# Optimization experiments

Measured on AMD Instinct MI355X. Metric: run time of the kernel, lower is better.

The kernel has to match this reference:

```python
import jax, jax.numpy as jnp
from jax import lax
import numpy as np

H = 256

def _cell(x, h, c, wih, whh, bih, bhh):
    # PyTorch LSTMCell: gates ordered i, f, g, o
    g = x @ wih.T + bih + h @ whh.T + bhh
    i, f, gg, o = jnp.split(g, 4, axis=-1)
    c = jax.nn.sigmoid(f) * c + jax.nn.sigmoid(i) * jnp.tanh(gg)
    h = jax.nn.sigmoid(o) * jnp.tanh(c)
    return h, c


def setup_inputs() -> dict:
    key = jax.random.key(0)
    ks = iter(jax.random.split(key, 64))
    def lin(out_f, in_f):
        s = 1.0 / np.sqrt(in_f)
        w = jax.random.uniform(next(ks), (out_f, in_f), minval=-s, maxval=s, dtype=jnp.float32)
        b = jax.random.uniform(next(ks), (out_f,), minval=-s, maxval=s, dtype=jnp.float32)
        return w, b
    def cellp():
        s = 1.0 / np.sqrt(H)
        return tuple(jax.random.uniform(next(ks), sh, minval=-s, maxval=s, dtype=jnp.float32)
                     for sh in [(4 * H, H), (4 * H, H), (4 * H,), (4 * H,)])
    d = {}
    d['x'] = jax.random.normal(next(ks), (20, 256, 64, 64), dtype=jnp.float32)
    d['fc_en1_w'], d['fc_en1_b'] = lin(1024, 4096)
    d['fc_en2_w'], d['fc_en2_b'] = lin(H, 1024)
    for nm in ['en1', 'en2', 'en3', 'de1', 'de2', 'de3']:
        d[nm + '_wih'], d[nm + '_whh'], d[nm + '_bih'], d[nm + '_bhh'] = cellp()
    d['fc_de1_w'], d['fc_de1_b'] = lin(1024, H)
    d['fc_de2_w'], d['fc_de2_b'] = lin(4096, 1024)
    d['future_step'] = 10
    return d


def reference(x, fc_en1_w, fc_en1_b, fc_en2_w, fc_en2_b,
              en1_wih, en1_whh, en1_bih, en1_bhh,
              en2_wih, en2_whh, en2_bih, en2_bhh,
              en3_wih, en3_whh, en3_bih, en3_bhh,
              de1_wih, de1_whh, de1_bih, de1_bhh,
              de2_wih, de2_whh, de2_bih, de2_bhh,
              de3_wih, de3_whh, de3_bih, de3_bhh,
              fc_de1_w, fc_de1_b, fc_de2_w, fc_de2_b, future_step):
    seq, B = x.shape[0], x.shape[1]
    xf = x.reshape(seq, B, -1)  # (S, B, 4096)
    z0 = jnp.zeros((B, H), x.dtype)

    def enc_step(carry, xt):
        h1, c1, h2, c2, h3, c3 = carry
        z = jax.nn.relu(xt @ fc_en1_w.T + fc_en1_b)
        z = jax.nn.relu(z @ fc_en2_w.T + fc_en2_b)
        h1, c1 = _cell(z, h1, c1, en1_wih, en1_whh, en1_bih, en1_bhh)
        h2, c2 = _cell(h1, h2, c2, en2_wih, en2_whh, en2_bih, en2_bhh)
        h3, c3 = _cell(h2, h3, c3, en3_wih, en3_whh, en3_bih, en3_bhh)
        return (h1, c1, h2, c2, h3, c3), None

    enc_carry, _ = lax.scan(enc_step, (z0,) * 6, xf)
    h_e3 = enc_carry[4]

    def dec_step(carry, _):
        h1, c1, h2, c2, h3, c3 = carry
        h1, c1 = _cell(z0, h1, c1, de1_wih, de1_whh, de1_bih, de1_bhh)
        h2, c2 = _cell(h1, h2, c2, de2_wih, de2_whh, de2_bih, de2_bhh)
        h3, c3 = _cell(h2, h3, c3, de3_wih, de3_whh, de3_bih, de3_bhh)
        y = jax.nn.relu(h3 @ fc_de1_w.T + fc_de1_b)
        y = jnp.tanh(y @ fc_de2_w.T + fc_de2_b)
        return (h1, c1, h2, c2, h3, c3), y

    _, ys = lax.scan(dec_step, (h_e3, z0, z0, z0, z0, z0), None, length=future_step)
    return ys.reshape(future_step, B, 64, 64)
```

## Files before the change

kernel.cpp:

```cpp
#include <hip/hip_runtime.h>
#include <math.h>

static __device__ __forceinline__ float sigf(float v) { return 1.0f / (1.0f + expf(-v)); }

using s8v = __attribute__((ext_vector_type(8))) short;
using f4v = __attribute__((ext_vector_type(4))) float;

static __device__ __forceinline__ void splitf(float f, unsigned short& h, unsigned short& l) {
  unsigned u = __float_as_uint(f);
  unsigned short hb = (unsigned short)((u + 0x7FFFu + ((u >> 16) & 1u)) >> 16);
  float hf = __uint_as_float(((unsigned)hb) << 16);
  float lf = f - hf;
  unsigned ul = __float_as_uint(lf);
  unsigned short lb = (unsigned short)((ul + 0x7FFFu + ((ul >> 16) & 1u)) >> 16);
  h = hb; l = lb;
}

static __device__ __forceinline__ void splitf4(float4 a, uint2& hOut, uint2& lOut) {
  unsigned hxy, hzw;
  asm("v_cvt_pk_bf16_f32 %0, %1, %2" : "=v"(hxy) : "v"(a.x), "v"(a.y));
  asm("v_cvt_pk_bf16_f32 %0, %1, %2" : "=v"(hzw) : "v"(a.z), "v"(a.w));
  float hx = __uint_as_float(hxy << 16);
  float hy = __uint_as_float(hxy & 0xFFFF0000u);
  float hz = __uint_as_float(hzw << 16);
  float hw = __uint_as_float(hzw & 0xFFFF0000u);
  unsigned lxy, lzw;
  asm("v_cvt_pk_bf16_f32 %0, %1, %2" : "=v"(lxy) : "v"(a.x - hx), "v"(a.y - hy));
  asm("v_cvt_pk_bf16_f32 %0, %1, %2" : "=v"(lzw) : "v"(a.z - hz), "v"(a.w - hw));
  hOut.x = hxy; hOut.y = hzw;
  lOut.x = lxy; lOut.y = lzw;
}

struct WsplitArgs {
  const float* W[4];
  unsigned short* WH[4];
  unsigned short* WL[4];
};
__global__ __launch_bounds__(256) void wsplit4(WsplitArgs a)
{
  int blk = blockIdx.x;
  int seg, base;
  if (blk < 4096)      { seg = 0; base = blk; }
  else if (blk < 4352) { seg = 1; base = blk - 4096; }
  else if (blk < 4608) { seg = 2; base = blk - 4352; }
  else                 { seg = 3; base = blk - 4608; }
  int i = base * 256 + threadIdx.x;
  float4 v = ((const float4*)a.W[seg])[i];
  ushort4 h, l;
  splitf(v.x, h.x, l.x); splitf(v.y, h.y, l.y);
  splitf(v.z, h.z, l.z); splitf(v.w, h.w, l.w);
  ((ushort4*)a.WH[seg])[i] = h;
  ((ushort4*)a.WL[seg])[i] = l;
}

template <int OSPLIT>
__global__ __launch_bounds__(256) void gemm_sf(
    const float* __restrict__ A,
    const unsigned short* __restrict__ WH, const unsigned short* __restrict__ WL,
    const float* __restrict__ bias, float* __restrict__ C,
    unsigned short* __restrict__ OH, unsigned short* __restrict__ OL,
    int M, int N, int K, int act)
{
  __shared__ unsigned short AsH[128 * 40];
  __shared__ unsigned short AsL[128 * 40];
  __shared__ unsigned short WsH[64 * 40];
  __shared__ unsigned short WsL[64 * 40];

  const int t = threadIdx.x;
  const int w = t >> 6, lane = t & 63;
  const int lrow = lane & 15, lk = (lane >> 4) * 8;
  const int m0 = blockIdx.x * 128, n0 = blockIdx.y * 64;

  f4v acc[2][4];
#pragma unroll
  for (int i = 0; i < 2; ++i)
#pragma unroll
    for (int j = 0; j < 4; ++j) acc[i][j] = (f4v){0.f, 0.f, 0.f, 0.f};

  for (int k0 = 0; k0 < K; k0 += 32) {
#pragma unroll
    for (int i = 0; i < 4; ++i) {
      int v = i * 256 + t;
      int row = v >> 3, kq = (v & 7) << 2;
      float4 a = *(const float4*)(A + (size_t)(m0 + row) * K + k0 + kq);
      uint2 h2, l2;
      splitf4(a, h2, l2);
      *(uint2*)&AsH[row * 40 + kq] = h2;
      *(uint2*)&AsL[row * 40 + kq] = l2;
    }
    {
      int row = t >> 2, q = (t & 3) * 8;
      *(s8v*)&WsH[row * 40 + q] = *(const s8v*)(WH + (size_t)(n0 + row) * K + k0 + q);
      *(s8v*)&WsL[row * 40 + q] = *(const s8v*)(WL + (size_t)(n0 + row) * K + k0 + q);
    }
    __syncthreads();

    s8v aH[2], aL[2], bH[4], bL[4];
#pragma unroll
    for (int mt = 0; mt < 2; ++mt) {
      int r = (w * 32 + mt * 16 + lrow) * 40 + lk;
      aH[mt] = *(const s8v*)&AsH[r];
      aL[mt] = *(const s8v*)&AsL[r];
    }
#pragma unroll
    for (int nt = 0; nt < 4; ++nt) {
      int r = (nt * 16 + lrow) * 40 + lk;
      bH[nt] = *(const s8v*)&WsH[r];
      bL[nt] = *(const s8v*)&WsL[r];
    }
#pragma unroll
    for (int mt = 0; mt < 2; ++mt)
#pragma unroll
      for (int nt = 0; nt < 4; ++nt) {
        acc[mt][nt] = __builtin_amdgcn_mfma_f32_16x16x32_bf16(aH[mt], bH[nt], acc[mt][nt], 0, 0, 0);
        acc[mt][nt] = __builtin_amdgcn_mfma_f32_16x16x32_bf16(aH[mt], bL[nt], acc[mt][nt], 0, 0, 0);
        acc[mt][nt] = __builtin_amdgcn_mfma_f32_16x16x32_bf16(aL[mt], bH[nt], acc[mt][nt], 0, 0, 0);
      }
    __syncthreads();
  }

#pragma unroll
  for (int mt = 0; mt < 2; ++mt)
#pragma unroll
    for (int nt = 0; nt < 4; ++nt) {
      int gcol = n0 + nt * 16 + lrow;
      float bv = bias[gcol];
#pragma unroll
      for (int r = 0; r < 4; ++r) {
        int grow = m0 + w * 32 + mt * 16 + (lane >> 4) * 4 + r;
        float v = acc[mt][nt][r] + bv;
        if (act == 1) v = fmaxf(v, 0.f);
        else if (act == 2) v = tanhf(v);
        if (OSPLIT) {
          unsigned short h, l;
          splitf(v, h, l);
          OH[(size_t)grow * N + gcol] = h;
          OL[(size_t)grow * N + gcol] = l;
        } else {
          C[(size_t)grow * N + gcol] = v;
        }
      }
    }
}

template <int OSPLIT>
__global__ __launch_bounds__(256) void gemm_bb(
    const unsigned short* __restrict__ AH, const unsigned short* __restrict__ AL,
    const unsigned short* __restrict__ WH, const unsigned short* __restrict__ WL,
    const float* __restrict__ bias, float* __restrict__ C,
    unsigned short* __restrict__ OH, unsigned short* __restrict__ OL,
    int M, int N, int K, int act)
{
  __shared__ unsigned short AsH[128 * 40];
  __shared__ unsigned short AsL[128 * 40];
  __shared__ unsigned short WsH[64 * 40];
  __shared__ unsigned short WsL[64 * 40];

  const int t = threadIdx.x;
  const int w = t >> 6, lane = t & 63;
  const int lrow = lane & 15, lk = (lane >> 4) * 8;
  const int m0 = blockIdx.x * 128, n0 = blockIdx.y * 64;

  f4v acc[2][4];
#pragma unroll
  for (int i = 0; i < 2; ++i)
#pragma unroll
    for (int j = 0; j < 4; ++j) acc[i][j] = (f4v){0.f, 0.f, 0.f, 0.f};

  for (int k0 = 0; k0 < K; k0 += 32) {
#pragma unroll
    for (int i = 0; i < 2; ++i) {
      int v = i * 256 + t;
      int row = v >> 2, q = (v & 3) * 8;
      *(s8v*)&AsH[row * 40 + q] = *(const s8v*)(AH + (size_t)(m0 + row) * K + k0 + q);
      *(s8v*)&AsL[row * 40 + q] = *(const s8v*)(AL + (size_t)(m0 + row) * K + k0 + q);
    }
    {
      int row = t >> 2, q = (t & 3) * 8;
      *(s8v*)&WsH[row * 40 + q] = *(const s8v*)(WH + (size_t)(n0 + row) * K + k0 + q);
      *(s8v*)&WsL[row * 40 + q] = *(const s8v*)(WL + (size_t)(n0 + row) * K + k0 + q);
    }
    __syncthreads();

    s8v aH[2], aL[2], bH[4], bL[4];
#pragma unroll
    for (int mt = 0; mt < 2; ++mt) {
      int r = (w * 32 + mt * 16 + lrow) * 40 + lk;
      aH[mt] = *(const s8v*)&AsH[r];
      aL[mt] = *(const s8v*)&AsL[r];
    }
#pragma unroll
    for (int nt = 0; nt < 4; ++nt) {
      int r = (nt * 16 + lrow) * 40 + lk;
      bH[nt] = *(const s8v*)&WsH[r];
      bL[nt] = *(const s8v*)&WsL[r];
    }
#pragma unroll
    for (int mt = 0; mt < 2; ++mt)
#pragma unroll
      for (int nt = 0; nt < 4; ++nt) {
        acc[mt][nt] = __builtin_amdgcn_mfma_f32_16x16x32_bf16(aH[mt], bH[nt], acc[mt][nt], 0, 0, 0);
        acc[mt][nt] = __builtin_amdgcn_mfma_f32_16x16x32_bf16(aH[mt], bL[nt], acc[mt][nt], 0, 0, 0);
        acc[mt][nt] = __builtin_amdgcn_mfma_f32_16x16x32_bf16(aL[mt], bH[nt], acc[mt][nt], 0, 0, 0);
      }
    __syncthreads();
  }

#pragma unroll
  for (int mt = 0; mt < 2; ++mt)
#pragma unroll
    for (int nt = 0; nt < 4; ++nt) {
      int gcol = n0 + nt * 16 + lrow;
      float bv = bias[gcol];
#pragma unroll
      for (int r = 0; r < 4; ++r) {
        int grow = m0 + w * 32 + mt * 16 + (lane >> 4) * 4 + r;
        float v = acc[mt][nt][r] + bv;
        if (act == 1) v = fmaxf(v, 0.f);
        else if (act == 2) v = tanhf(v);
        if (OSPLIT) {
          unsigned short h, l;
          splitf(v, h, l);
          OH[(size_t)grow * N + gcol] = h;
          OL[(size_t)grow * N + gcol] = l;
        } else {
          C[(size_t)grow * N + gcol] = v;
        }
      }
    }
}

struct PrepArgs {
  const float* wih[6];
  const float* whh[6];
  const float* bih[6];
  const float* bhh[6];
  float* wihP;
  float* whhP;
  float* bP;
};
__global__ __launch_bounds__(256) void prep_pack6(PrepArgs a)
{
  const int l = blockIdx.y;
  const int j = blockIdx.x, k = threadIdx.x;
  const float* wih = a.wih[l];
  const float* whh = a.whh[l];
  float* wihP = a.wihP + (size_t)l * 262144;
  float* whhP = a.whhP + (size_t)l * 262144;
  float4 v, c;
  v.x = wih[(0 * 256 + j) * 256 + k];
  v.y = wih[(1 * 256 + j) * 256 + k];
  v.z = wih[(2 * 256 + j) * 256 + k];
  v.w = wih[(3 * 256 + j) * 256 + k];
  *(float4*)&wihP[((size_t)j * 256 + k) * 4] = v;
  c.x = whh[(0 * 256 + j) * 256 + k];
  c.y = whh[(1 * 256 + j) * 256 + k];
  c.z = whh[(2 * 256 + j) * 256 + k];
  c.w = whh[(3 * 256 + j) * 256 + k];
  *(float4*)&whhP[((size_t)j * 256 + k) * 4] = c;
  if (k < 4)
    a.bP[l * 1024 + j * 4 + k] = a.bih[l][k * 256 + j] + a.bhh[l][k * 256 + j];
}

__global__ __launch_bounds__(256) void transpose256(
    const float* __restrict__ in, float* __restrict__ out)
{
  const int t = blockIdx.x, c4 = blockIdx.y;
  const int r = threadIdx.x;
  float4 v = *(const float4*)(in + ((size_t)t * 256 + r) * 256 + c4 * 4);
  float* op = out + (size_t)t * 65536 + (size_t)(c4 * 4) * 256 + r;
  op[0]   = v.x;
  op[256] = v.y;
  op[512] = v.z;
  op[768] = v.w;
}

__global__ __launch_bounds__(256) void transpose256s(
    const float* __restrict__ in, unsigned short* __restrict__ outH,
    unsigned short* __restrict__ outL)
{
  const int t = blockIdx.x, c4 = blockIdx.y;
  const int r = threadIdx.x;
  float4 v = *(const float4*)(in + ((size_t)t * 256 + r) * 256 + c4 * 4);
  ushort4 h, l;
  splitf(v.x, h.x, l.x); splitf(v.y, h.y, l.y);
  splitf(v.z, h.z, l.z); splitf(v.w, h.w, l.w);
  size_t o = (size_t)t * 65536 + (size_t)(c4 * 4) * 256 + r;
  outH[o] = h.x; outH[o + 256] = h.y; outH[o + 512] = h.z; outH[o + 768] = h.w;
  outL[o] = l.x; outL[o + 256] = l.y; outL[o + 512] = l.z; outL[o + 768] = l.w;
}

struct CellSlot {
  const float* x;
  const float* wih;
  const float* whh;
  const float* bias;
  const float* hin;
  float* c;
  float* hout;
  float* hcopy;
  int hasx;
};
struct CellArgs { CellSlot s[3]; };

__global__ __launch_bounds__(512) void cell_multi(CellArgs args)
{
  __shared__ float part[4][64][4];
  const CellSlot S = args.s[blockIdx.x >> 8];
  const int inner = blockIdx.x & 255;
  const int jg = inner & 63, bg = inner >> 6;
  const int t = threadIdx.x;
  const int lane = t & 63;
  const int wave = t >> 6;
  const int jwv = wave & 3;
  const int kh = __builtin_amdgcn_readfirstlane(wave >> 2);
  const int b = bg * 64 + lane;

  const int jw = __builtin_amdgcn_readfirstlane(jg * 4 + jwv);
  const float4* wh = (const float4*)(S.whh + (size_t)jw * 1024) + kh * 128;
  const float4* wi = (const float4*)(S.wih + (size_t)jw * 1024) + kh * 128;
  const float* hcol = S.hin + (size_t)kh * 128 * 256 + b;

  float4 acc;
  if (kh == 0) acc = *(const float4*)(S.bias + jw * 4);
  else         acc = (float4){0.f, 0.f, 0.f, 0.f};

  if (S.hasx) {
    const float* xcol = S.x + (size_t)kh * 128 * 256 + b;
#pragma unroll 8
    for (int k = 0; k < 128; ++k) {
      const float hv = hcol[k * 256];
      const float4 wv = wh[k];
      acc.x = fmaf(hv, wv.x, acc.x);
      acc.y = fmaf(hv, wv.y, acc.y);
      acc.z = fmaf(hv, wv.z, acc.z);
      acc.w = fmaf(hv, wv.w, acc.w);
      const float xv = xcol[k * 256];
      const float4 vv = wi[k];
      acc.x = fmaf(xv, vv.x, acc.x);
      acc.y = fmaf(xv, vv.y, acc.y);
      acc.z = fmaf(xv, vv.z, acc.z);
      acc.w = fmaf(xv, vv.w, acc.w);
    }
  } else {
#pragma unroll 8
    for (int k = 0; k < 128; ++k) {
      const float hv = hcol[k * 256];
      const float4 wv = wh[k];
      acc.x = fmaf(hv, wv.x, acc.x);
      acc.y = fmaf(hv, wv.y, acc.y);
      acc.z = fmaf(hv, wv.z, acc.z);
      acc.w = fmaf(hv, wv.w, acc.w);
    }
  }

  if (kh == 1) *(float4*)&part[jwv][lane][0] = acc;
  __syncthreads();
  if (kh == 0) {
    const float4 p = *(const float4*)&part[jwv][lane][0];
    acc.x += p.x; acc.y += p.y; acc.z += p.z; acc.w += p.w;

    const int idx = jw * 256 + b;
    const float cold = S.c[idx];
    const float ig = sigf(acc.x), fg = sigf(acc.y);
    const float gg = tanhf(acc.z), og = sigf(acc.w);
    const float cn = fg * cold + ig * gg;
    const float hn = og * tanhf(cn);
    S.c[idx] = cn;
    S.hout[idx] = hn;
    if (S.hcopy) S.hcopy[idx] = hn;
  }
}


extern "C" void kernel_launch(void* const* d_in, const int* in_sizes, int n_in,
                              void* d_out, int out_size, void* d_ws, size_t ws_size,
                              hipStream_t stream)
{
  const float* x_in  = (const float*)d_in[0];
  const float* w_en1 = (const float*)d_in[1];
  const float* b_en1 = (const float*)d_in[2];
  const float* w_en2 = (const float*)d_in[3];
  const float* b_en2 = (const float*)d_in[4];
  const float* cw[6][4];
  for (int i = 0; i < 6; ++i)
    for (int j = 0; j < 4; ++j) cw[i][j] = (const float*)d_in[5 + i * 4 + j];
  const float* w_de1 = (const float*)d_in[29];
  const float* b_de1 = (const float*)d_in[30];
  const float* w_de2 = (const float*)d_in[31];
  const float* b_de2 = (const float*)d_in[32];
  float* out = (float*)d_out;

  float* fs   = (float*)d_ws;
  float* wihP = fs;
  float* whhP = wihP + 6 * 262144;
  float* bP   = whhP + 6 * 262144;
  float* hb   = bP + 6 * 1024;
  float* cb   = hb + 12 * 65536;
  float* H3T  = cb + 6 * 65536;
  float* z2   = H3T + 10 * 65536;
  float* z2T  = z2 + 1310720;
  unsigned short* us = (unsigned short*)(z2T + 1310720);
  unsigned short* WEN1H = us;              us += 4194304;
  unsigned short* WEN1L = us;              us += 4194304;
  unsigned short* WEN2H = us;              us += 262144;
  unsigned short* WEN2L = us;              us += 262144;
  unsigned short* WDE1H = us;              us += 262144;
  unsigned short* WDE1L = us;              us += 262144;
  unsigned short* WDE2H = us;              us += 4194304;
  unsigned short* WDE2L = us;              us += 4194304;
  unsigned short* Z1H   = us;              us += 5242880;
  unsigned short* Z1L   = us;              us += 5242880;
  unsigned short* H3H = Z1H;
  unsigned short* H3L = Z1H + 655360;
  unsigned short* Y1H = Z1H + 1310720;
  unsigned short* Y1L = Z1H + 1310720 + 2621440;

  PrepArgs pa;
  for (int i = 0; i < 6; ++i) {
    pa.wih[i] = cw[i][0]; pa.whh[i] = cw[i][1];
    pa.bih[i] = cw[i][2]; pa.bhh[i] = cw[i][3];
  }
  pa.wihP = wihP; pa.whhP = whhP; pa.bP = bP;
  prep_pack6<<<dim3(256, 6), 256, 0, stream>>>(pa);

  WsplitArgs wa;
  wa.W[0] = w_en1; wa.WH[0] = WEN1H; wa.WL[0] = WEN1L;
  wa.W[1] = w_en2; wa.WH[1] = WEN2H; wa.WL[1] = WEN2L;
  wa.W[2] = w_de1; wa.WH[2] = WDE1H; wa.WL[2] = WDE1L;
  wa.W[3] = w_de2; wa.WH[3] = WDE2H; wa.WL[3] = WDE2L;
  wsplit4<<<8704, 256, 0, stream>>>(wa);
  hipMemsetAsync(hb, 0, (size_t)18 * 65536 * sizeof(float), stream);

  gemm_sf<1><<<dim3(40, 16), 256, 0, stream>>>(
      x_in, WEN1H, WEN1L, b_en1, nullptr, Z1H, Z1L, 5120, 1024, 4096, 1);
  gemm_bb<0><<<dim3(40, 4), 256, 0, stream>>>(
      Z1H, Z1L, WEN2H, WEN2L, b_en2, z2, nullptr, nullptr, 5120, 256, 1024, 1);
  transpose256<<<dim3(20, 64), 256, 0, stream>>>(z2, z2T);

  int pp[6] = {0, 0, 0, 0, 0, 0};
  auto HBuf = [&](int l, int p) { return hb + (size_t)(l * 2 + p) * 65536; };
  auto CBuf = [&](int l) { return cb + (size_t)l * 65536; };
  auto WI = [&](int l) { return wihP + (size_t)l * 262144; };
  auto WHp = [&](int l) { return whhP + (size_t)l * 262144; };
  auto BB = [&](int l) { return bP + (size_t)l * 1024; };

  for (int s = 0; s <= 21; ++s) {
    CellArgs a; int n = 0; int tog[3]; int nt = 0;
    if (s < 20) {
      a.s[n++] = {z2T + (size_t)s * 65536, WI(0), WHp(0), BB(0),
                  HBuf(0, pp[0]), CBuf(0), HBuf(0, pp[0] ^ 1), nullptr, 1};
      tog[nt++] = 0;
    }
    if (s >= 1 && s <= 20) {
      a.s[n++] = {HBuf(0, pp[0]), WI(1), WHp(1), BB(1),
                  HBuf(1, pp[1]), CBuf(1), HBuf(1, pp[1] ^ 1), nullptr, 1};
      tog[nt++] = 1;
    }
    if (s >= 2) {
      a.s[n++] = {HBuf(1, pp[1]), WI(2), WHp(2), BB(2),
                  HBuf(2, pp[2]), CBuf(2), HBuf(2, pp[2] ^ 1), nullptr, 1};
      tog[nt++] = 2;
    }
    cell_multi<<<n * 256, 512, 0, stream>>>(a);
    for (int i = 0; i < nt; ++i) pp[tog[i]] ^= 1;
  }

  for (int s = 0; s <= 11; ++s) {
    CellArgs a; int n = 0; int tog[3]; int nt = 0;
    if (s < 10) {
      const float* h1in = (s == 0) ? HBuf(2, pp[2]) : HBuf(3, pp[3]);
      a.s[n++] = {nullptr, WI(3), WHp(3), BB(3),
                  h1in, CBuf(3), HBuf(3, pp[3] ^ 1), nullptr, 0};
      tog[nt++] = 3;
    }
    if (s >= 1 && s <= 10) {
      a.s[n++] = {HBuf(3, pp[3]), WI(4), WHp(4), BB(4),
                  HBuf(4, pp[4]), CBuf(4), HBuf(4, pp[4] ^ 1), nullptr, 1};
      tog[nt++] = 4;
    }
    if (s >= 2) {
      a.s[n++] = {HBuf(4, pp[4]), WI(5), WHp(5), BB(5),
                  HBuf(5, pp[5]), CBuf(5), HBuf(5, pp[5] ^ 1),
                  H3T + (size_t)(s - 2) * 65536, 1};
      tog[nt++] = 5;
    }
    cell_multi<<<n * 256, 512, 0, stream>>>(a);
    for (int i = 0; i < nt; ++i) pp[tog[i]] ^= 1;
  }

  transpose256s<<<dim3(10, 64), 256, 0, stream>>>(H3T, H3H, H3L);
  gemm_bb<1><<<dim3(20, 16), 256, 0, stream>>>(
      H3H, H3L, WDE1H, WDE1L, b_de1, nullptr, Y1H, Y1L, 2560, 1024, 256, 1);
  gemm_bb<0><<<dim3(20, 64), 256, 0, stream>>>(
      Y1H, Y1L, WDE2H, WDE2L, b_de2, out, nullptr, nullptr, 2560, 4096, 1024, 2);

  (void)in_sizes; (void)n_in; (void)out_size; (void)ws_size;
}
```

Before: 844.5 us.

## Run LSTM cell recurrences on split-bf16 MFMA with concatenated weights

Replaces the scalar FP32 FMA LSTM cell kernel with an MFMA-based kernel that multiplies a concatenated [Whh|Wih] bf16 hi/lo split weight matrix against hi/lo split hidden/input states, emulating FP32 precision with three bf16 MFMAs. Hidden states are now stored as bf16 hi/lo pairs in batch-major layout, which removes the separate transpose kernels and lets the encoder fc2 output feed the cells directly. The intent is to cut the per-step latency of the 34 sequential cell launches by using matrix cores. The trade-off is that the launch now uses only 32 blocks per layer, which leaves most of the GPU idle, and the three-term split drops the lo*lo product, so precision is slightly lower.

Measured after the change: 933.3 us. 1.11x slower.

```diff
diff --git a/kernel.cpp b/kernel.cpp
--- a/kernel.cpp
+++ b/kernel.cpp
@@ -53,6 +53,37 @@
   ((ushort4*)a.WL[seg])[i] = l;
 }
 
+struct PrepArgs {
+  const float* wih[6];
+  const float* whh[6];
+  const float* bih[6];
+  const float* bhh[6];
+  unsigned short* WcatH;
+  unsigned short* WcatL;
+  float* bP;
+};
+__global__ __launch_bounds__(256) void prep_cat6(PrepArgs a)
+{
+  const int l = blockIdx.y;
+  const int j = blockIdx.x, k = threadIdx.x;
+  unsigned short* WH = a.WcatH + (size_t)l * 524288;
+  unsigned short* WL = a.WcatL + (size_t)l * 524288;
+#pragma unroll
+  for (int s = 0; s < 4; ++s) {
+    unsigned short h, lo;
+    float wh = a.whh[l][(s * 256 + j) * 256 + k];
+    splitf(wh, h, lo);
+    WH[(size_t)(j * 4 + s) * 512 + k] = h;
+    WL[(size_t)(j * 4 + s) * 512 + k] = lo;
+    float wi = a.wih[l][(s * 256 + j) * 256 + k];
+    splitf(wi, h, lo);
+    WH[(size_t)(j * 4 + s) * 512 + 256 + k] = h;
+    WL[(size_t)(j * 4 + s) * 512 + 256 + k] = lo;
+  }
+  if (k < 4)
+    a.bP[l * 1024 + j * 4 + k] = a.bih[l][k * 256 + j] + a.bhh[l][k * 256 + j];
+}
+
 template <int OSPLIT>
 __global__ __launch_bounds__(256) void gemm_sf(
     const float* __restrict__ A,
@@ -230,145 +261,129 @@
     }
 }
 
-struct PrepArgs {
-  const float* wih[6];
-  const float* whh[6];
-  const float* bih[6];
-  const float* bhh[6];
-  float* wihP;
-  float* whhP;
-  float* bP;
+struct CSlot {
+  const unsigned short* wH;
+  const unsigned short* wL;
+  const float* bias;
+  const unsigned short* xH;
+  const unsigned short* xL;
+  const unsigned short* hH;
+  const unsigned short* hL;
+  float* c;
+  unsigned short* oH;
+  unsigned short* oL;
+  unsigned short* h3H;
+  unsigned short* h3L;
+  int h3off;
+  int K;
 };
-__global__ __launch_bounds__(256) void prep_pack6(PrepArgs a)
+struct CArgs { CSlot s[3]; };
+
+__global__ __launch_bounds__(256) void cell_mfma(CArgs args)
 {
-  const int l = blockIdx.y;
-  const int j = blockIdx.x, k = threadIdx.x;
-  const float* wih = a.wih[l];
-  const float* whh = a.whh[l];
-  float* wihP = a.wihP + (size_t)l * 262144;
-  float* whhP = a.whhP + (size_t)l * 262144;
-  float4 v, c;
-  v.x = wih[(0 * 256 + j) * 256 + k];
-  v.y = wih[(1 * 256 + j) * 256 + k];
-  v.z = wih[(2 * 256 + j) * 256 + k];
-  v.w = wih[(3 * 256 + j) * 256 + k];
-  *(float4*)&wihP[((size_t)j * 256 + k) * 4] = v;
-  c.x = whh[(0 * 256 + j) * 256 + k];
-  c.y = whh[(1 * 256 + j) * 256 + k];
-  c.z = whh[(2 * 256 + j) * 256 + k];
-  c.w = whh[(3 * 256 + j) * 256 + k];
-  *(float4*)&whhP[((size_t)j * 256 + k) * 4] = c;
-  if (k < 4)
-    a.bP[l * 1024 + j * 4 + k] = a.bih[l][k * 256 + j] + a.bhh[l][k * 256 + j];
-}
-
-__global__ __launch_bounds__(256) void transpose256(
-    const float* __restrict__ in, float* __restrict__ out)
-{
-  const int t = blockIdx.x, c4 = blockIdx.y;
-  const int r = threadIdx.x;
-  float4 v = *(const float4*)(in + ((size_t)t * 256 + r) * 256 + c4 * 4);
-  float* op = out + (size_t)t * 65536 + (size_t)(c4 * 4) * 256 + r;
-  op[0]   = v.x;
-  op[256] = v.y;
-  op[512] = v.z;
-  op[768] = v.w;
-}
-
-__global__ __launch_bounds__(256) void transpose256s(
-    const float* __restrict__ in, unsigned short* __restrict__ outH,
-    unsigned short* __restrict__ outL)
-{
-  const int t = blockIdx.x, c4 = blockIdx.y;
-  const int r = threadIdx.x;
-  float4 v = *(const float4*)(in + ((size_t)t * 256 + r) * 256 + c4 * 4);
-  ushort4 h, l;
-  splitf(v.x, h.x, l.x); splitf(v.y, h.y, l.y);
-  splitf(v.z, h.z, l.z); splitf(v.w, h.w, l.w);
-  size_t o = (size_t)t * 65536 + (size_t)(c4 * 4) * 256 + r;
-  outH[o] = h.x; outH[o + 256] = h.y; outH[o + 512] = h.z; outH[o + 768] = h.w;
-  outL[o] = l.x; outL[o + 256] = l.y; outL[o + 512] = l.z; outL[o + 768] = l.w;
-}
-
-struct CellSlot {
-  const float* x;
-  const float* wih;
-  const float* whh;
-  const float* bias;
-  const float* hin;
-  float* c;
-  float* hout;
-  float* hcopy;
-  int hasx;
-};
-struct CellArgs { CellSlot s[3]; };
-
-__global__ __launch_bounds__(512) void cell_multi(CellArgs args)
-{
-  __shared__ float part[4][64][4];
-  const CellSlot S = args.s[blockIdx.x >> 8];
-  const int inner = blockIdx.x & 255;
-  const int jg = inner & 63, bg = inner >> 6;
+  __shared__ unsigned short AsH[128 * 40];
+  __shared__ unsigned short AsL[128 * 40];
+  __shared__ unsigned short WsH[64 * 40];
+  __shared__ unsigned short WsL[64 * 40];
+  __shared__ unsigned short tH[64 * 34];
+  __shared__ unsigned short tL[64 * 34];
+
+  const CSlot S = args.s[blockIdx.x >> 5];
+  const int inner = blockIdx.x & 31;
+  const int m0 = (inner >> 2) * 128, n0 = (inner & 3) * 64;
   const int t = threadIdx.x;
-  const int lane = t & 63;
-  const int wave = t >> 6;
-  const int jwv = wave & 3;
-  const int kh = __builtin_amdgcn_readfirstlane(wave >> 2);
-  const int b = bg * 64 + lane;
-
-  const int jw = __builtin_amdgcn_readfirstlane(jg * 4 + jwv);
-  const float4* wh = (const float4*)(S.whh + (size_t)jw * 1024) + kh * 128;
-  const float4* wi = (const float4*)(S.wih + (size_t)jw * 1024) + kh * 128;
-  const float* hcol = S.hin + (size_t)kh * 128 * 256 + b;
-
-  float4 acc;
-  if (kh == 0) acc = *(const float4*)(S.bias + jw * 4);
-  else         acc = (float4){0.f, 0.f, 0.f, 0.f};
-
-  if (S.hasx) {
-    const float* xcol = S.x + (size_t)kh * 128 * 256 + b;
-#pragma unroll 8
-    for (int k = 0; k < 128; ++k) {
-      const float hv = hcol[k * 256];
-      const float4 wv = wh[k];
-      acc.x = fmaf(hv, wv.x, acc.x);
-      acc.y = fmaf(hv, wv.y, acc.y);
-      acc.z = fmaf(hv, wv.z, acc.z);
-      acc.w = fmaf(hv, wv.w, acc.w);
-      const float xv = xcol[k * 256];
-      const float4 vv = wi[k];
-      acc.x = fmaf(xv, vv.x, acc.x);
-      acc.y = fmaf(xv, vv.y, acc.y);
-      acc.z = fmaf(xv, vv.z, acc.z);
-      acc.w = fmaf(xv, vv.w, acc.w);
-    }
-  } else {
-#pragma unroll 8
-    for (int k = 0; k < 128; ++k) {
-      const float hv = hcol[k * 256];
-      const float4 wv = wh[k];
-      acc.x = fmaf(hv, wv.x, acc.x);
-      acc.y = fmaf(hv, wv.y, acc.y);
-      acc.z = fmaf(hv, wv.z, acc.z);
-      acc.w = fmaf(hv, wv.w, acc.w);
-    }
-  }
-
-  if (kh == 1) *(float4*)&part[jwv][lane][0] = acc;
+  const int w = t >> 6, lane = t & 63;
+  const int lrow = lane & 15, lk = (lane >> 4) * 8;
+
+  f4v acc[2][4];
+#pragma unroll
+  for (int i = 0; i < 2; ++i)
+#pragma unroll
+    for (int j = 0; j < 4; ++j) acc[i][j] = (f4v){0.f, 0.f, 0.f, 0.f};
+
+  for (int k0 = 0; k0 < S.K; k0 += 32) {
+#pragma unroll
+    for (int i = 0; i < 2; ++i) {
+      int v = i * 256 + t;
+      int row = v >> 2, q = (v & 3) * 8;
+      *(s8v*)&AsH[row * 40 + q] = *(const s8v*)(S.wH + (size_t)(m0 + row) * 512 + k0 + q);
+      *(s8v*)&AsL[row * 40 + q] = *(const s8v*)(S.wL + (size_t)(m0 + row) * 512 + k0 + q);
+    }
+    {
+      const unsigned short* bh = (k0 < 256) ? (S.hH + k0) : (S.xH + (k0 - 256));
+      const unsigned short* bl = (k0 < 256) ? (S.hL + k0) : (S.xL + (k0 - 256));
+      int row = t >> 2, q = (t & 3) * 8;
+      *(s8v*)&WsH[row * 40 + q] = *(const s8v*)(bh + (size_t)(n0 + row) * 256 + q);
+      *(s8v*)&WsL[row * 40 + q] = *(const s8v*)(bl + (size_t)(n0 + row) * 256 + q);
+    }
+    __syncthreads();
+
+    s8v aH[2], aL[2], bH[4], bL[4];
+#pragma unroll
+    for (int mt = 0; mt < 2; ++mt) {
+      int r = (w * 32 + mt * 16 + lrow) * 40 + lk;
+      aH[mt] = *(const s8v*)&AsH[r];
+      aL[mt] = *(const s8v*)&AsL[r];
+    }
+#pragma unroll
+    for (int nt = 0; nt < 4; ++nt) {
+      int r = (nt * 16 + lrow) * 40 + lk;
+      bH[nt] = *(const s8v*)&WsH[r];
+      bL[nt] = *(const s8v*)&WsL[r];
+    }
+#pragma unroll
+    for (int mt = 0; mt < 2; ++mt)
+#pragma unroll
+      for (int nt = 0; nt < 4; ++nt) {
+        acc[mt][nt] = __builtin_amdgcn_mfma_f32_16x16x32_bf16(aH[mt], bH[nt], acc[mt][nt], 0, 0, 0);
+        acc[mt][nt] = __builtin_amdgcn_mfma_f32_16x16x32_bf16(aH[mt], bL[nt], acc[mt][nt], 0, 0, 0);
+        acc[mt][nt] = __builtin_amdgcn_mfma_f32_16x16x32_bf16(aL[mt], bH[nt], acc[mt][nt], 0, 0, 0);
+      }
+    __syncthreads();
+  }
+
+#pragma unroll
+  for (int mt = 0; mt < 2; ++mt)
+#pragma unroll
+    for (int nt = 0; nt < 4; ++nt) {
+      const int gbase = m0 + w * 32 + mt * 16 + (lane >> 4) * 4;
+      const int j = gbase >> 2;
+      const int b = n0 + nt * 16 + lrow;
+      const float4 bv = *(const float4*)(S.bias + gbase);
+      const float ig = sigf(acc[mt][nt][0] + bv.x);
+      const float fg = sigf(acc[mt][nt][1] + bv.y);
+      const float gg = tanhf(acc[mt][nt][2] + bv.z);
+      const float og = sigf(acc[mt][nt][3] + bv.w);
+      const int idx = j * 256 + b;
+      const float cn = fg * S.c[idx] + ig * gg;
+      const float hn = og * tanhf(cn);
+      S.c[idx] = cn;
+      unsigned short hh, hl;
+      splitf(hn, hh, hl);
+      const int jl = w * 8 + mt * 4 + (lane >> 4);
+      const int bl = nt * 16 + lrow;
+      tH[bl * 34 + jl] = hh;
+      tL[bl * 34 + jl] = hl;
+    }
   __syncthreads();
-  if (kh == 0) {
-    const float4 p = *(const float4*)&part[jwv][lane][0];
-    acc.x += p.x; acc.y += p.y; acc.z += p.z; acc.w += p.w;
-
-    const int idx = jw * 256 + b;
-    const float cold = S.c[idx];
-    const float ig = sigf(acc.x), fg = sigf(acc.y);
-    const float gg = tanhf(acc.z), og = sigf(acc.w);
-    const float cn = fg * cold + ig * gg;
-    const float hn = og * tanhf(cn);
-    S.c[idx] = cn;
-    S.hout[idx] = hn;
-    if (S.hcopy) S.hcopy[idx] = hn;
+
+  {
+    const int row = t >> 2, seg = t & 3;
+    const int j0 = m0 >> 2;
+    unsigned short vh[8], vl[8];
+#pragma unroll
+    for (int q = 0; q < 8; ++q) {
+      vh[q] = tH[row * 34 + seg * 8 + q];
+      vl[q] = tL[row * 34 + seg * 8 + q];
+    }
+    size_t o = (size_t)(n0 + row) * 256 + j0 + seg * 8;
+    *(s8v*)(S.oH + o) = *(const s8v*)vh;
+    *(s8v*)(S.oL + o) = *(const s8v*)vl;
+    if (S.h3H) {
+      size_t o3 = (size_t)(S.h3off + n0 + row) * 256 + j0 + seg * 8;
+      *(s8v*)(S.h3H + o3) = *(const s8v*)vh;
+      *(s8v*)(S.h3L + o3) = *(const s8v*)vl;
+    }
   }
 }
 
@@ -391,16 +406,14 @@
   const float* b_de2 = (const float*)d_in[32];
   float* out = (float*)d_out;
 
-  float* fs   = (float*)d_ws;
-  float* wihP = fs;
-  float* whhP = wihP + 6 * 262144;
-  float* bP   = whhP + 6 * 262144;
-  float* hb   = bP + 6 * 1024;
-  float* cb   = hb + 12 * 65536;
-  float* H3T  = cb + 6 * 65536;
-  float* z2   = H3T + 10 * 65536;
-  float* z2T  = z2 + 1310720;
-  unsigned short* us = (unsigned short*)(z2T + 1310720);
+  float* fs = (float*)d_ws;
+  float* bP = fs;
+  float* cb = bP + 6 * 1024;
+  unsigned short* us = (unsigned short*)(cb + 6 * 65536);
+  unsigned short* hbH   = us;              us += 12 * 65536;
+  unsigned short* hbL   = us;              us += 12 * 65536;
+  unsigned short* WcatH = us;              us += 6 * 524288;
+  unsigned short* WcatL = us;              us += 6 * 524288;
   unsigned short* WEN1H = us;              us += 4194304;
   unsigned short* WEN1L = us;              us += 4194304;
   unsigned short* WEN2H = us;              us += 262144;
@@ -411,18 +424,20 @@
   unsigned short* WDE2L = us;              us += 4194304;
   unsigned short* Z1H   = us;              us += 5242880;
   unsigned short* Z1L   = us;              us += 5242880;
-  unsigned short* H3H = Z1H;
-  unsigned short* H3L = Z1H + 655360;
-  unsigned short* Y1H = Z1H + 1310720;
-  unsigned short* Y1L = Z1H + 1310720 + 2621440;
+  unsigned short* Z2H   = us;              us += 1310720;
+  unsigned short* Z2L   = us;              us += 1310720;
+  unsigned short* H3H   = us;              us += 655360;
+  unsigned short* H3L   = us;              us += 655360;
+  unsigned short* Y1H   = us;              us += 2621440;
+  unsigned short* Y1L   = us;              us += 2621440;
 
   PrepArgs pa;
   for (int i = 0; i < 6; ++i) {
     pa.wih[i] = cw[i][0]; pa.whh[i] = cw[i][1];
     pa.bih[i] = cw[i][2]; pa.bhh[i] = cw[i][3];
   }
-  pa.wihP = wihP; pa.whhP = whhP; pa.bP = bP;
-  prep_pack6<<<dim3(256, 6), 256, 0, stream>>>(pa);
+  pa.WcatH = WcatH; pa.WcatL = WcatL; pa.bP = bP;
+  prep_cat6<<<dim3(256, 6), 256, 0, stream>>>(pa);
 
   WsplitArgs wa;
   wa.W[0] = w_en1; wa.WH[0] = WEN1H; wa.WL[0] = WEN1L;
@@ -430,66 +445,83 @@
   wa.W[2] = w_de1; wa.WH[2] = WDE1H; wa.WL[2] = WDE1L;
   wa.W[3] = w_de2; wa.WH[3] = WDE2H; wa.WL[3] = WDE2L;
   wsplit4<<<8704, 256, 0, stream>>>(wa);
-  hipMemsetAsync(hb, 0, (size_t)18 * 65536 * sizeof(float), stream);
+  hipMemsetAsync(cb, 0, (size_t)6 * 65536 * 4 + (size_t)24 * 65536 * 2, stream);
 
   gemm_sf<1><<<dim3(40, 16), 256, 0, stream>>>(
       x_in, WEN1H, WEN1L, b_en1, nullptr, Z1H, Z1L, 5120, 1024, 4096, 1);
-  gemm_bb<0><<<dim3(40, 4), 256, 0, stream>>>(
-      Z1H, Z1L, WEN2H, WEN2L, b_en2, z2, nullptr, nullptr, 5120, 256, 1024, 1);
-  transpose256<<<dim3(20, 64), 256, 0, stream>>>(z2, z2T);
+  gemm_bb<1><<<dim3(40, 4), 256, 0, stream>>>(
+      Z1H, Z1L, WEN2H, WEN2L, b_en2, nullptr, Z2H, Z2L, 5120, 256, 1024, 1);
 
   int pp[6] = {0, 0, 0, 0, 0, 0};
-  auto HBuf = [&](int l, int p) { return hb + (size_t)(l * 2 + p) * 65536; };
-  auto CBuf = [&](int l) { return cb + (size_t)l * 65536; };
-  auto WI = [&](int l) { return wihP + (size_t)l * 262144; };
-  auto WHp = [&](int l) { return whhP + (size_t)l * 262144; };
+  auto HH = [&](int l, int p) { return hbH + (size_t)(l * 2 + p) * 65536; };
+  auto HL = [&](int l, int p) { return hbL + (size_t)(l * 2 + p) * 65536; };
+  auto CBf = [&](int l) { return cb + (size_t)l * 65536; };
+  auto WCH = [&](int l) { return WcatH + (size_t)l * 524288; };
+  auto WCL = [&](int l) { return WcatL + (size_t)l * 524288; };
   auto BB = [&](int l) { return bP + (size_t)l * 1024; };
 
   for (int s = 0; s <= 21; ++s) {
-    CellArgs a; int n = 0; int tog[3]; int nt = 0;
+    CArgs a; int n = 0; int tog[3]; int nt = 0;
     if (s < 20) {
-      a.s[n++] = {z2T + (size_t)s * 65536, WI(0), WHp(0), BB(0),
-                  HBuf(0, pp[0]), CBuf(0), HBuf(0, pp[0] ^ 1), nullptr, 1};
+      a.s[n++] = {WCH(0), WCL(0), BB(0),
+                  Z2H + (size_t)s * 65536, Z2L + (size_t)s * 65536,
+                  HH(0, pp[0]), HL(0, pp[0]), CBf(0),
+                  HH(0, pp[0] ^ 1), HL(0, pp[0] ^ 1),
+                  nullptr, nullptr, 0, 512};
       tog[nt++] = 0;
     }
     if (s >= 1 && s <= 20) {
-      a.s[n++] = {HBuf(0, pp[0]), WI(1), WHp(1), BB(1),
-                  HBuf(1, pp[1]), CBuf(1), HBuf(1, pp[1] ^ 1), nullptr, 1};
+      a.s[n++] = {WCH(1), WCL(1), BB(1),
+                  HH(0, pp[0]), HL(0, pp[0]),
+                  HH(1, pp[1]), HL(1, pp[1]), CBf(1),
+                  HH(1, pp[1] ^ 1), HL(1, pp[1] ^ 1),
+                  nullptr, nullptr, 0, 512};
       tog[nt++] = 1;
     }
     if (s >= 2) {
-      a.s[n++] = {HBuf(1, pp[1]), WI(2), WHp(2), BB(2),
-                  HBuf(2, pp[2]), CBuf(2), HBuf(2, pp[2] ^ 1), nullptr, 1};
+      a.s[n++] = {WCH(2), WCL(2), BB(2),
+                  HH(1, pp[1]), HL(1, pp[1]),
+                  HH(2, pp[2]), HL(2, pp[2]), CBf(2),
+                  HH(2, pp[2] ^ 1), HL(2, pp[2] ^ 1),
+                  nullptr, nullptr, 0, 512};
       tog[nt++] = 2;
     }
-    cell_multi<<<n * 256, 512, 0, stream>>>(a);
+    cell_mfma<<<n * 32, 256, 0, stream>>>(a);
     for (int i = 0; i < nt; ++i) pp[tog[i]] ^= 1;
   }
 
   for (int s = 0; s <= 11; ++s) {
-    CellArgs a; int n = 0; int tog[3]; int nt = 0;
+    CArgs a; int n = 0; int tog[3]; int nt = 0;
     if (s < 10) {
-      const float* h1in = (s == 0) ? HBuf(2, pp[2]) : HBuf(3, pp[3]);
-      a.s[n++] = {nullptr, WI(3), WHp(3), BB(3),
-                  h1in, CBuf(3), HBuf(3, pp[3] ^ 1), nullptr, 0};
+      const unsigned short* h1H = (s == 0) ? HH(2, pp[2]) : HH(3, pp[3]);
+      const unsigned short* h1L = (s == 0) ? HL(2, pp[2]) : HL(3, pp[3]);
+      a.s[n++] = {WCH(3), WCL(3), BB(3),
+                  nullptr, nullptr,
+                  h1H, h1L, CBf(3),
+                  HH(3, pp[3] ^ 1), HL(3, pp[3] ^ 1),
+                  nullptr, nullptr, 0, 256};
       tog[nt++] = 3;
     }
     if (s >= 1 && s <= 10) {
-      a.s[n++] = {HBuf(3, pp[3]), WI(4), WHp(4), BB(4),
-                  HBuf(4, pp[4]), CBuf(4), HBuf(4, pp[4] ^ 1), nullptr, 1};
+      a.s[n++] = {WCH(4), WCL(4), BB(4),
+                  HH(3, pp[3]), HL(3, pp[3]),
+                  HH(4, pp[4]), HL(4, pp[4]), CBf(4),
+                  HH(4, pp[4] ^ 1), HL(4, pp[4] ^ 1),
+                  nullptr, nullptr, 0, 512};
       tog[nt++] = 4;
     }
     if (s >= 2) {
-      a.s[n++] = {HBuf(4, pp[4]), WI(5), WHp(5), BB(5),
-                  HBuf(5, pp[5]), CBuf(5), HBuf(5, pp[5] ^ 1),
-                  H3T + (size_t)(s - 2) * 65536, 1};
+      a.s[n++] = {WCH(5), WCL(5), BB(5),
+                  HH(4, pp[4]), HL(4, pp[4]),
+                  HH(5, pp[5]), HL(5, pp[5]), CBf(5),
+                  HH(5, pp[5] ^ 1), HL(5, pp[5] ^ 1),
+                  H3H, H3L, (s - 2) * 256, 512};
       tog[nt++] = 5;
     }
-    cell_multi<<<n * 256, 512, 0, stream>>>(a);
+    cell_mfma<<<n * 32, 256, 0, stream>>>(a);
     for (int i = 0; i < nt; ++i) pp[tog[i]] ^= 1;
   }
 
-  transpose256s<<<dim3(10, 64), 256, 0, stream>>>(H3T, H3H, H3L);
   gemm_bb<1><<<dim3(20, 16), 256, 0, stream>>>(
       H3H, H3L, WDE1H, WDE1L, b_de1, nullptr, Y1H, Y1L, 2560, 1024, 256, 1);
   gemm_bb<0><<<dim3(20, 64), 256, 0, stream>>>(
```
